# Performance work log

Hardware: AMD Instinct MI355X
Metric: run time of the kernel (lower is better)

The kernel has to match this reference:

```python
import jax, jax.numpy as jnp
import numpy as np

N_EMBD = 1024
N_HEAD = 16
HEAD_SIZE = 64

def setup_inputs() -> dict:
    key = jax.random.key(0)
    ks = jax.random.split(key, 6)
    B, T = 4, 2048
    x = jax.random.normal(ks[0], (B, T, N_EMBD), dtype=jnp.float32)
    s = 1.0 / np.sqrt(N_EMBD)
    Wq = jax.random.normal(ks[1], (N_HEAD, N_EMBD, HEAD_SIZE), dtype=jnp.float32) * s
    Wk = jax.random.normal(ks[2], (N_HEAD, N_EMBD, HEAD_SIZE), dtype=jnp.float32) * s
    Wv = jax.random.normal(ks[3], (N_HEAD, N_EMBD, HEAD_SIZE), dtype=jnp.float32) * s
    Wp = jax.random.normal(ks[4], (N_EMBD, N_EMBD), dtype=jnp.float32) * s
    bp = jax.random.normal(ks[5], (N_EMBD,), dtype=jnp.float32) * 0.01
    return {"x": x, "Wq": Wq, "Wk": Wk, "Wv": Wv, "Wp": Wp, "bp": bp}

def reference(x, Wq, Wk, Wv, Wp, bp):
    B, T, C = x.shape
    # per-head projections, all heads at once: [B,H,T,hs]
    q = jnp.einsum('btc,hcd->bhtd', x, Wq)
    k = jnp.einsum('btc,hcd->bhtd', x, Wk)
    v = jnp.einsum('btc,hcd->bhtd', x, Wv)
    # NOTE: original scales by C**-0.5 with C = n_embd (not head_size)
    scale = C ** (-0.5)
    wei = jnp.einsum('bhtd,bhsd->bhts', q, k) * scale  # [B,H,T,T]
    causal = jnp.tril(jnp.ones((T, T), dtype=bool))
    wei = jnp.where(causal, wei, -jnp.inf)
    wei = jax.nn.softmax(wei, axis=-1)
    out = jnp.einsum('bhts,bhsd->bhtd', wei, v)  # [B,H,T,hs]
    out = out.transpose(0, 2, 1, 3).reshape(B, T, -1)  # concat heads -> [B,T,C]
    return out @ Wp + bp
```

## Files before the change

kernel.cpp:

```cpp
#include <hip/hip_runtime.h>
#include <stdint.h>
#include <math.h>

typedef short s16x8 __attribute__((ext_vector_type(8)));
typedef float f32x4 __attribute__((ext_vector_type(4)));
typedef float f32x16 __attribute__((ext_vector_type(16)));

__device__ __forceinline__ unsigned short f2bf(float f) {
    union { float f; uint32_t u; } x; x.f = f;
    uint32_t r = x.u + 0x7FFFu + ((x.u >> 16) & 1u);
    return (unsigned short)(r >> 16);
}

__device__ __forceinline__ uint32_t cvtpk_bf16(float lo, float hi) {
    uint32_t r;
    asm("v_cvt_pk_bf16_f32 %0, %1, %2" : "=v"(r) : "v"(lo), "v"(hi));
    return r;
}

#define GLD_LDS16(gp, lp) __builtin_amdgcn_global_load_lds( \
    (const __attribute__((address_space(1))) uint32_t*)(gp), \
    (__attribute__((address_space(3))) uint32_t*)(lp), 16, 0, 0)

#define MFMA16x16x32(a, b, c) __builtin_amdgcn_mfma_f32_16x16x32_bf16((a), (b), (c), 0, 0, 0)
#define MFMA32x32x16(a, b, c) __builtin_amdgcn_mfma_f32_32x32x16_bf16((a), (b), (c), 0, 0, 0)

__device__ __forceinline__ void plswap(uint32_t a, uint32_t b, int lh, uint32_t& x, uint32_t& y) {
#if __has_builtin(__builtin_amdgcn_permlane32_swap)
    auto r = __builtin_amdgcn_permlane32_swap(a, b, false, false);
    x = (uint32_t)r[0]; y = (uint32_t)r[1];
#else
    uint32_t as = (uint32_t)__shfl_xor((int)a, 32, 64);
    uint32_t bs = (uint32_t)__shfl_xor((int)b, 32, 64);
    x = lh ? bs : a;
    y = lh ? b : as;
#endif
}

__global__ void cvt_all_kernel(const float* __restrict__ x,
                               const float* __restrict__ Wq, const float* __restrict__ Wk,
                               const float* __restrict__ Wv, const float* __restrict__ Wp,
                               unsigned short* __restrict__ xb,
                               unsigned short* __restrict__ WtQKV, unsigned short* __restrict__ WtP,
                               int xunits) {
    int u = blockIdx.x * blockDim.x + threadIdx.x;
    if (u < xunits) {
        int i = u * 4;
        float4 v = *(const float4*)(x + i);
        unsigned short o0 = f2bf(v.x), o1 = f2bf(v.y), o2 = f2bf(v.z), o3 = f2bf(v.w);
        uint64_t packed = (uint64_t)o0 | ((uint64_t)o1 << 16) | ((uint64_t)o2 << 32) | ((uint64_t)o3 << 48);
        *(uint64_t*)(xb + i) = packed;
        return;
    }
    int id = (u - xunits) * 4;
    int which = id >> 20, rem = id & 1048575;
    const float* src = (which == 0) ? Wq : (which == 1) ? Wk : (which == 2) ? Wv : Wp;
    float4 v = *(const float4*)(src + rem);
    unsigned short* dst;
    if (which < 3) {
        int h = rem >> 16, c = (rem >> 6) & 1023, d = rem & 63;
        dst = WtQKV + (size_t)(which * 1024 + h * 64 + d) * 1024 + c;
    } else {
        int c = rem >> 10, n = rem & 1023;
        dst = WtP + (size_t)n * 1024 + c;
    }
    dst[0] = f2bf(v.x); dst[1024] = f2bf(v.y); dst[2048] = f2bf(v.z); dst[3072] = f2bf(v.w);
}

template<int MODE, int CPX>
__global__ __launch_bounds__(512, 4) void gemm_dp_kernel(
    const unsigned short* __restrict__ A, const unsigned short* __restrict__ Bt,
    void* __restrict__ Cout, unsigned short* __restrict__ vT,
    const float* __restrict__ bias)
{
    constexpr int K = 1024, NT = 32;
    __shared__ __align__(16) unsigned short LA[3][128 * 32];
    __shared__ __align__(16) unsigned short LB[3][256 * 32];

    const int t = threadIdx.x, w = t >> 6, l = t & 63, lr = l & 15, lg = l >> 4;
    const int wm2 = w >> 2, wn4 = w & 3;

    int bid = blockIdx.x;
    int swz = (bid & 7) * CPX + (bid >> 3);
    const int bm = (swz & 63) << 7, bn = (swz >> 6) << 8;

    const unsigned short* Ab = A + (size_t)bm * K;
    const unsigned short* Bb = Bt + (size_t)bn * K;

    int sArow, sAce, sBrow[2], sBce[2];
    {
        int u = t >> 4, x = (t & 15) ^ (u & 15);
        sArow = 4 * u + (x >> 2); sAce = (x & 3) << 3;
        #pragma unroll
        for (int i2 = 0; i2 < 2; ++i2) {
            int i = t + i2 * 512;
            int ub = i >> 4, xb2 = (i & 15) ^ (ub & 15);
            sBrow[i2] = 4 * ub + (xb2 >> 2); sBce[i2] = (xb2 & 3) << 3;
        }
    }

    int aoff[4], boff[4];
    #pragma unroll
    for (int m = 0; m < 4; ++m) {
        int u = 16 * wm2 + 4 * m + (lr >> 2);
        aoff[m] = u * 256 + (((lg + 4 * (lr & 3)) ^ (u & 15)) << 4);
    }
    #pragma unroll
    for (int n = 0; n < 4; ++n) {
        int u = 16 * wn4 + 4 * n + (lr >> 2);
        boff[n] = u * 256 + (((lg + 4 * (lr & 3)) ^ (u & 15)) << 4);
    }

    f32x4 acc[4][4] = {};

    GLD_LDS16(Ab + (size_t)sArow * K + 0 + sAce, &LA[0][t * 8]);
    #pragma unroll
    for (int i2 = 0; i2 < 2; ++i2)
        GLD_LDS16(Bb + (size_t)sBrow[i2] * K + 0 + sBce[i2], &LB[0][(t + i2 * 512) * 8]);
    GLD_LDS16(Ab + (size_t)sArow * K + 32 + sAce, &LA[1][t * 8]);
    #pragma unroll
    for (int i2 = 0; i2 < 2; ++i2)
        GLD_LDS16(Bb + (size_t)sBrow[i2] * K + 32 + sBce[i2], &LB[1][(t + i2 * 512) * 8]);
    asm volatile("s_waitcnt vmcnt(3)" ::: "memory");
    __builtin_amdgcn_sched_barrier(0);
    __builtin_amdgcn_s_barrier();

    int cur = 0;
    for (int j = 0; j < NT; ++j) {
        const int dst = (cur >= 1) ? cur - 1 : cur + 2;
        const bool st = (j + 2 < NT);
        const int k2 = (j + 2) << 5;
        s16x8 af[4], bfr[4];
        #pragma unroll
        for (int m = 0; m < 4; ++m)
            af[m] = *(const s16x8*)((const char*)LA[cur] + aoff[m]);
        #pragma unroll
        for (int n = 0; n < 4; ++n)
            bfr[n] = *(const s16x8*)((const char*)LB[cur] + boff[n]);
        if (st) {
            GLD_LDS16(Ab + (size_t)sArow * K + k2 + sAce, &LA[dst][t * 8]);
            #pragma unroll
            for (int i2 = 0; i2 < 2; ++i2)
                GLD_LDS16(Bb + (size_t)sBrow[i2] * K + k2 + sBce[i2], &LB[dst][(t + i2 * 512) * 8]);
        }
        __builtin_amdgcn_s_barrier();
        asm volatile("s_waitcnt lgkmcnt(0)" ::: "memory");
        __builtin_amdgcn_sched_barrier(0);
        __builtin_amdgcn_s_setprio(1);
        #pragma unroll
        for (int m = 0; m < 4; ++m)
            #pragma unroll
            for (int n = 0; n < 4; ++n)
                acc[m][n] = MFMA16x16x32(af[m], bfr[n], acc[m][n]);
        __builtin_amdgcn_s_setprio(0);
        if (j + 1 < NT) {
            if (st) { asm volatile("s_waitcnt vmcnt(3)" ::: "memory"); }
            else    { asm volatile("s_waitcnt vmcnt(0)" ::: "memory"); }
            __builtin_amdgcn_sched_barrier(0);
        }
        __builtin_amdgcn_s_barrier();
        cur = (cur == 2) ? 0 : cur + 1;
    }

    if (MODE == 1) {
        float* C = (float*)Cout;
        #pragma unroll
        for (int mi = 0; mi < 4; ++mi)
            #pragma unroll
            for (int ni = 0; ni < 4; ++ni) {
                int col = bn + wn4 * 64 + ni * 16 + lr;
                float bv = bias[col];
                int row0 = bm + wm2 * 64 + mi * 16 + lg * 4;
                #pragma unroll
                for (int r = 0; r < 4; ++r)
                    C[(size_t)(row0 + r) * 1024 + col] = acc[mi][ni][r] + bv;
            }
    } else {
        unsigned short* qkv2 = (unsigned short*)Cout;
        const bool isV = (bn >= 2048);
        const float sc = (bn < 1024) ? (0.03125f * 1.44269504088896341f) : 1.0f;
        #pragma unroll
        for (int mi = 0; mi < 4; ++mi)
            #pragma unroll
            for (int ni = 0; ni < 4; ++ni) {
                int col = bn + wn4 * 64 + ni * 16 + lr;
                int row0 = bm + wm2 * 64 + mi * 16 + lg * 4;
                if (!isV) {
                    #pragma unroll
                    for (int r = 0; r < 4; ++r)
                        qkv2[(size_t)(row0 + r) * 2048 + col] = f2bf(acc[mi][ni][r] * sc);
                } else {
                    int h = (col >> 6) & 15, d = col & 63;
                    size_t vb = ((size_t)((row0 >> 11) * 16 + h) * 64 + d) * 2048 + (row0 & 2047);
                    uint32_t u0 = (uint32_t)f2bf(acc[mi][ni][0]) | ((uint32_t)f2bf(acc[mi][ni][1]) << 16);
                    uint32_t u1 = (uint32_t)f2bf(acc[mi][ni][2]) | ((uint32_t)f2bf(acc[mi][ni][3]) << 16);
                    *(uint32_t*)&vT[vb]     = u0;
                    *(uint32_t*)&vT[vb + 2] = u1;
                }
            }
    }
}

__device__ __forceinline__ void proc32(
    const unsigned short* __restrict__ Ksb, const unsigned short* __restrict__ Vtb,
    const s16x8* qf, f32x16* o, float& m_r, f32x16& l_acc, s16x8 onesf,
    int qms, bool domask, int lq, int lh)
{
    const int ub = lq >> 1;
    const int vb8 = (lq & 1) << 3;
    f32x16 S[2] = {};
    __builtin_amdgcn_s_setprio(1);
    #pragma unroll
    for (int sblk = 0; sblk < 2; ++sblk)
        #pragma unroll
        for (int kd = 0; kd < 4; ++kd) {
            s16x8 kf = *(const s16x8*)((const char*)Ksb + (sblk * 16 + ub) * 256
                                       + ((((2 * kd + lh) + vb8) ^ ub) << 4));
            S[sblk] = MFMA32x32x16(kf, qf[kd], S[sblk]);
        }
    __builtin_amdgcn_s_setprio(0);
    if (domask) {
        #pragma unroll
        for (int sblk = 0; sblk < 2; ++sblk)
            #pragma unroll
            for (int r = 0; r < 16; ++r) {
                int s_loc = sblk * 32 + (r & 3) + 8 * (r >> 2) + 4 * lh;
                S[sblk][r] = (s_loc <= qms) ? S[sblk][r] : -1e30f;
            }
    }
    float zm = S[0][0];
    #pragma unroll
    for (int r = 1; r < 15; r += 2) zm = fmaxf(fmaxf(zm, S[0][r]), S[0][r + 1]);
    zm = fmaxf(zm, S[0][15]);
    #pragma unroll
    for (int r = 0; r < 16; r += 2) zm = fmaxf(fmaxf(zm, S[1][r]), S[1][r + 1]);
    zm = fmaxf(zm, __shfl_xor(zm, 32, 64));
    const bool defer = (__all(zm <= m_r + 8.0f) != 0);
    if (!defer) {
        float mn = fmaxf(m_r, zm);
        float alpha = exp2f(m_r - mn);
        m_r = mn;
        l_acc[0] *= alpha;
        o[0] *= alpha;
        o[1] *= alpha;
    }
    uint32_t pk[2][8];
    #pragma unroll
    for (int sblk = 0; sblk < 2; ++sblk) {
        #pragma unroll
        for (int r = 0; r < 16; ++r)
            S[sblk][r] = exp2f(S[sblk][r] - m_r);
        #pragma unroll
        for (int hh = 0; hh < 8; ++hh)
            pk[sblk][hh] = cvtpk_bf16(S[sblk][2 * hh], S[sblk][2 * hh + 1]);
    }
    s16x8 pf[4];
    #pragma unroll
    for (int ks2 = 0; ks2 < 4; ++ks2) {
        int sb = ks2 >> 1, Bh = 4 * (ks2 & 1);
        uint32_t w0, w1, w2, w3;
        plswap(pk[sb][Bh + 0], pk[sb][Bh + 2], lh, w0, w2);
        plswap(pk[sb][Bh + 1], pk[sb][Bh + 3], lh, w1, w3);
        union { uint32_t u[4]; s16x8 v; } pu;
        pu.u[0] = w0; pu.u[1] = w1; pu.u[2] = w2; pu.u[3] = w3;
        pf[ks2] = pu.v;
    }
    __builtin_amdgcn_s_setprio(1);
    #pragma unroll
    for (int dblk = 0; dblk < 2; ++dblk)
        #pragma unroll
        for (int ks2 = 0; ks2 < 4; ++ks2) {
            s16x8 vf = *(const s16x8*)((const char*)Vtb + (dblk * 16 + ub) * 256
                                       + ((((2 * ks2 + lh) + vb8) ^ ub) << 4));
            o[dblk] = MFMA32x32x16(vf, pf[ks2], o[dblk]);
        }
    #pragma unroll
    for (int ks2 = 0; ks2 < 4; ++ks2)
        l_acc = MFMA32x32x16(onesf, pf[ks2], l_acc);
    __builtin_amdgcn_s_setprio(0);
}

__global__ __launch_bounds__(256, 4) void attn_kernel(
    const unsigned short* __restrict__ qkv2, const unsigned short* __restrict__ vT,
    unsigned short* __restrict__ attnO, int T)
{
    __shared__ __align__(16) unsigned short Ks[2][64 * 64];
    __shared__ __align__(16) unsigned short Vt[2][64 * 64];

    const int i = blockIdx.x;
    const int g = i & 7, j = i >> 3;
    const int tq = 15 - (j >> 3);
    const int bh = ((j & 7) << 3) | g;
    const int b = bh >> 4, h = bh & 15;
    const int nkv = 2 * tq + 2;

    const int t = threadIdx.x, w = t >> 6, l = t & 63, lq = l & 31, lh = l >> 5;
    const int c0 = tq * 128 + 32 * w;
    const int lastT = (c0 + 31) >> 6;

    const unsigned short* qbase = qkv2 + (size_t)b * T * 2048;
    const unsigned short* kbase = qbase + 1024 + h * 64;
    const unsigned short* vtb   = vT + (size_t)(b * 16 + h) * 64 * 2048;

    s16x8 qf[4];
    #pragma unroll
    for (int kd = 0; kd < 4; ++kd)
        qf[kd] = *(const s16x8*)(qbase + (size_t)(c0 + lq) * 2048 + h * 64 + kd * 16 + lh * 8);

    f32x16 o[2] = {}, l_acc = {};
    float m_r = -1e30f;
    s16x8 onesf;
    {
        union { uint32_t u[4]; s16x8 v; } ou;
        #pragma unroll
        for (int k2 = 0; k2 < 4; ++k2) ou.u[k2] = 0x3F803F80u;
        onesf = ou.v;
    }

    int srow[2], sch[2];
    #pragma unroll
    for (int i2 = 0; i2 < 2; ++i2) {
        int c = t + i2 * 256;
        int su = c >> 4, sx = (c & 15) ^ (su & 15);
        srow[i2] = 2 * su + (sx >> 3); sch[i2] = (sx & 7) << 3;
    }
    auto STAGE = [&](int buf, int s0) {
        #pragma unroll
        for (int i2 = 0; i2 < 2; ++i2) {
            int c = t + i2 * 256;
            GLD_LDS16(kbase + (size_t)(s0 + srow[i2]) * 2048 + sch[i2], &Ks[buf][c * 8]);
            GLD_LDS16(vtb + (size_t)srow[i2] * 2048 + s0 + sch[i2], &Vt[buf][c * 8]);
        }
    };

    STAGE(0, 0);
    __syncthreads();

    for (int kt = 0; kt < nkv; ++kt) {
        const int cur = kt & 1, nxt = cur ^ 1;
        if (kt + 1 < nkv) STAGE(nxt, (kt + 1) * 64);
        if (kt <= lastT)
            proc32(Ks[cur], Vt[cur], qf, o, m_r, l_acc, onesf,
                   c0 + lq - kt * 64, kt == lastT, lq, lh);
        __syncthreads();
    }

    {
        float inv = 1.0f / l_acc[0];
        #pragma unroll
        for (int dblk = 0; dblk < 2; ++dblk)
            #pragma unroll
            for (int r = 0; r < 16; r += 2) {
                int d = dblk * 32 + (r & 3) + 8 * (r >> 2) + 4 * lh;
                uint32_t ua = cvtpk_bf16(o[dblk][r] * inv, o[dblk][r + 1] * inv);
                *(uint32_t*)&attnO[(size_t)(b * T + c0 + lq) * 1024 + h * 64 + d] = ua;
            }
    }
}

extern "C" void kernel_launch(void* const* d_in, const int* in_sizes, int n_in,
                              void* d_out, int out_size, void* d_ws, size_t ws_size,
                              hipStream_t stream) {
    const float* x  = (const float*)d_in[0];
    const float* Wq = (const float*)d_in[1];
    const float* Wk = (const float*)d_in[2];
    const float* Wv = (const float*)d_in[3];
    const float* Wp = (const float*)d_in[4];
    const float* bp = (const float*)d_in[5];
    float* out = (float*)d_out;

    const int T = 2048, C = 1024;
    const int BT = in_sizes[0] / C;
    const int B  = BT / T;

    char* ws = (char*)d_ws;
    unsigned short* xb    = (unsigned short*)(ws);
    unsigned short* WtQKV = (unsigned short*)(ws + 16777216);
    unsigned short* WtP   = (unsigned short*)(ws + 23068672);
    unsigned short* qkv2  = (unsigned short*)(ws + 25165824);
    unsigned short* vT    = (unsigned short*)(ws + 58720256);
    unsigned short* attn  = (unsigned short*)(ws + 75497472);
    (void)ws_size; (void)n_in; (void)out_size;

    const int xunits = BT * C / 4;
    const int wunits = 4 * 1024 * 1024 / 4;
    cvt_all_kernel<<<(xunits + wunits) / 256, 256, 0, stream>>>(
        x, Wq, Wk, Wv, Wp, xb, WtQKV, WtP, xunits);

    gemm_dp_kernel<0, 96><<<768, 512, 0, stream>>>(xb, WtQKV, qkv2, vT, nullptr);

    attn_kernel<<<B * 16 * 16, 256, 0, stream>>>(qkv2, vT, attn, T);

    gemm_dp_kernel<1, 32><<<256, 512, 0, stream>>>(attn, WtP, out, nullptr, bp);
}
```

Baseline: 198.4 us.

## Split attention KV tiles across wave pairs and merge partial softmax states

Each block now handles 64 queries instead of 128, so the grid doubles. Each pair of waves splits the 64-key tile into two 32-key halves, each half keeping its own running max and sum, and the halves are merged through LDS at the end. The row-sum MFMA against a ones vector is replaced by a scalar sum with a lane shuffle, and the occupancy hint rises from 4 to 5. This aims to cut causal load imbalance and per-tile MFMA work, at the cost of loading each K/V tile twice as often overall and adding an LDS merge epilogue.

```diff
diff --git a/kernel.cpp b/kernel.cpp
--- a/kernel.cpp
+++ b/kernel.cpp
@@ -201,102 +201,94 @@
     }
 }
 
-__device__ __forceinline__ void proc32(
+__device__ __forceinline__ void proc32h(
     const unsigned short* __restrict__ Ksb, const unsigned short* __restrict__ Vtb,
-    const s16x8* qf, f32x16* o, float& m_r, f32x16& l_acc, s16x8 onesf,
-    int qms, bool domask, int lq, int lh)
+    const s16x8* qf, f32x16* o, float& m_r, float& l_r,
+    int qms, bool domask, int lq, int lh, int wp)
 {
     const int ub = lq >> 1;
     const int vb8 = (lq & 1) << 3;
-    f32x16 S[2] = {};
+    f32x16 S = {};
     __builtin_amdgcn_s_setprio(1);
     #pragma unroll
-    for (int sblk = 0; sblk < 2; ++sblk)
-        #pragma unroll
-        for (int kd = 0; kd < 4; ++kd) {
-            s16x8 kf = *(const s16x8*)((const char*)Ksb + (sblk * 16 + ub) * 256
-                                       + ((((2 * kd + lh) + vb8) ^ ub) << 4));
-            S[sblk] = MFMA32x32x16(kf, qf[kd], S[sblk]);
-        }
+    for (int kd = 0; kd < 4; ++kd) {
+        s16x8 kf = *(const s16x8*)((const char*)Ksb + (wp * 16 + ub) * 256
+                                   + ((((2 * kd + lh) + vb8) ^ ub) << 4));
+        S = MFMA32x32x16(kf, qf[kd], S);
+    }
     __builtin_amdgcn_s_setprio(0);
     if (domask) {
         #pragma unroll
-        for (int sblk = 0; sblk < 2; ++sblk)
-            #pragma unroll
-            for (int r = 0; r < 16; ++r) {
-                int s_loc = sblk * 32 + (r & 3) + 8 * (r >> 2) + 4 * lh;
-                S[sblk][r] = (s_loc <= qms) ? S[sblk][r] : -1e30f;
-            }
-    }
-    float zm = S[0][0];
-    #pragma unroll
-    for (int r = 1; r < 15; r += 2) zm = fmaxf(fmaxf(zm, S[0][r]), S[0][r + 1]);
-    zm = fmaxf(zm, S[0][15]);
-    #pragma unroll
-    for (int r = 0; r < 16; r += 2) zm = fmaxf(fmaxf(zm, S[1][r]), S[1][r + 1]);
+        for (int r = 0; r < 16; ++r) {
+            int s_loc = (r & 3) + 8 * (r >> 2) + 4 * lh;
+            S[r] = (s_loc <= qms) ? S[r] : -1e30f;
+        }
+    }
+    float zm = fmaxf(S[0], S[1]);
+    #pragma unroll
+    for (int r = 2; r < 16; r += 2) zm = fmaxf(fmaxf(zm, S[r]), S[r + 1]);
     zm = fmaxf(zm, __shfl_xor(zm, 32, 64));
     const bool defer = (__all(zm <= m_r + 8.0f) != 0);
     if (!defer) {
         float mn = fmaxf(m_r, zm);
         float alpha = exp2f(m_r - mn);
         m_r = mn;
-        l_acc[0] *= alpha;
+        l_r *= alpha;
         o[0] *= alpha;
         o[1] *= alpha;
     }
-    uint32_t pk[2][8];
-    #pragma unroll
-    for (int sblk = 0; sblk < 2; ++sblk) {
-        #pragma unroll
-        for (int r = 0; r < 16; ++r)
-            S[sblk][r] = exp2f(S[sblk][r] - m_r);
-        #pragma unroll
-        for (int hh = 0; hh < 8; ++hh)
-            pk[sblk][hh] = cvtpk_bf16(S[sblk][2 * hh], S[sblk][2 * hh + 1]);
-    }
-    s16x8 pf[4];
-    #pragma unroll
-    for (int ks2 = 0; ks2 < 4; ++ks2) {
-        int sb = ks2 >> 1, Bh = 4 * (ks2 & 1);
+    float rs = 0.0f;
+    uint32_t pk[8];
+    #pragma unroll
+    for (int r = 0; r < 16; ++r) {
+        float pv = exp2f(S[r] - m_r);
+        S[r] = pv;
+        rs += pv;
+    }
+    #pragma unroll
+    for (int hh = 0; hh < 8; ++hh)
+        pk[hh] = cvtpk_bf16(S[2 * hh], S[2 * hh + 1]);
+    rs += __shfl_xor(rs, 32, 64);
+    l_r += rs;
+    s16x8 pf[2];
+    #pragma unroll
+    for (int jj = 0; jj < 2; ++jj) {
         uint32_t w0, w1, w2, w3;
-        plswap(pk[sb][Bh + 0], pk[sb][Bh + 2], lh, w0, w2);
-        plswap(pk[sb][Bh + 1], pk[sb][Bh + 3], lh, w1, w3);
+        plswap(pk[4 * jj + 0], pk[4 * jj + 2], lh, w0, w2);
+        plswap(pk[4 * jj + 1], pk[4 * jj + 3], lh, w1, w3);
         union { uint32_t u[4]; s16x8 v; } pu;
         pu.u[0] = w0; pu.u[1] = w1; pu.u[2] = w2; pu.u[3] = w3;
-        pf[ks2] = pu.v;
+        pf[jj] = pu.v;
     }
     __builtin_amdgcn_s_setprio(1);
     #pragma unroll
     for (int dblk = 0; dblk < 2; ++dblk)
         #pragma unroll
-        for (int ks2 = 0; ks2 < 4; ++ks2) {
+        for (int jj = 0; jj < 2; ++jj) {
+            int kc = 2 * (2 * wp + jj) + lh;
             s16x8 vf = *(const s16x8*)((const char*)Vtb + (dblk * 16 + ub) * 256
-                                       + ((((2 * ks2 + lh) + vb8) ^ ub) << 4));
-            o[dblk] = MFMA32x32x16(vf, pf[ks2], o[dblk]);
-        }
-    #pragma unroll
-    for (int ks2 = 0; ks2 < 4; ++ks2)
-        l_acc = MFMA32x32x16(onesf, pf[ks2], l_acc);
+                                       + (((kc + vb8) ^ ub) << 4));
+            o[dblk] = MFMA32x32x16(vf, pf[jj], o[dblk]);
+        }
     __builtin_amdgcn_s_setprio(0);
 }
 
-__global__ __launch_bounds__(256, 4) void attn_kernel(
+__global__ __launch_bounds__(256, 5) void attn_kernel(
     const unsigned short* __restrict__ qkv2, const unsigned short* __restrict__ vT,
     unsigned short* __restrict__ attnO, int T)
 {
-    __shared__ __align__(16) unsigned short Ks[2][64 * 64];
-    __shared__ __align__(16) unsigned short Vt[2][64 * 64];
+    __shared__ __align__(16) unsigned short SMEM[4][64 * 64];
 
     const int i = blockIdx.x;
     const int g = i & 7, j = i >> 3;
-    const int tq = 15 - (j >> 3);
+    const int tq = 31 - (j >> 3);
     const int bh = ((j & 7) << 3) | g;
     const int b = bh >> 4, h = bh & 15;
-    const int nkv = 2 * tq + 2;
+    const int nkv = tq + 1;
 
     const int t = threadIdx.x, w = t >> 6, l = t & 63, lq = l & 31, lh = l >> 5;
-    const int c0 = tq * 128 + 32 * w;
-    const int lastT = (c0 + 31) >> 6;
+    const int ws = w & 1, wp = w >> 1;
+    const int c0 = tq * 64 + 32 * ws;
 
     const unsigned short* qbase = qkv2 + (size_t)b * T * 2048;
     const unsigned short* kbase = qbase + 1024 + h * 64;
@@ -307,15 +299,8 @@
     for (int kd = 0; kd < 4; ++kd)
         qf[kd] = *(const s16x8*)(qbase + (size_t)(c0 + lq) * 2048 + h * 64 + kd * 16 + lh * 8);
 
-    f32x16 o[2] = {}, l_acc = {};
-    float m_r = -1e30f;
-    s16x8 onesf;
-    {
-        union { uint32_t u[4]; s16x8 v; } ou;
-        #pragma unroll
-        for (int k2 = 0; k2 < 4; ++k2) ou.u[k2] = 0x3F803F80u;
-        onesf = ou.v;
-    }
+    f32x16 o[2] = {};
+    float m_r = -1e30f, l_r = 0.0f;
 
     int srow[2], sch[2];
     #pragma unroll
@@ -328,8 +313,8 @@
         #pragma unroll
         for (int i2 = 0; i2 < 2; ++i2) {
             int c = t + i2 * 256;
-            GLD_LDS16(kbase + (size_t)(s0 + srow[i2]) * 2048 + sch[i2], &Ks[buf][c * 8]);
-            GLD_LDS16(vtb + (size_t)srow[i2] * 2048 + s0 + sch[i2], &Vt[buf][c * 8]);
+            GLD_LDS16(kbase + (size_t)(s0 + srow[i2]) * 2048 + sch[i2], &SMEM[buf][c * 8]);
+            GLD_LDS16(vtb + (size_t)srow[i2] * 2048 + s0 + sch[i2], &SMEM[2 + buf][c * 8]);
         }
     };
 
@@ -339,20 +324,41 @@
     for (int kt = 0; kt < nkv; ++kt) {
         const int cur = kt & 1, nxt = cur ^ 1;
         if (kt + 1 < nkv) STAGE(nxt, (kt + 1) * 64);
-        if (kt <= lastT)
-            proc32(Ks[cur], Vt[cur], qf, o, m_r, l_acc, onesf,
-                   c0 + lq - kt * 64, kt == lastT, lq, lh);
+        const int sbase = 64 * kt + 32 * wp;
+        if (sbase <= c0 + 31)
+            proc32h(SMEM[cur], SMEM[2 + cur], qf, o, m_r, l_r,
+                    c0 + lq - sbase, sbase + 31 > c0, lq, lh, wp);
         __syncthreads();
     }
 
-    {
-        float inv = 1.0f / l_acc[0];
+    float* fs = (float*)&SMEM[0][0];
+    if (lh == 0) { fs[w * 64 + lq * 2] = m_r; fs[w * 64 + lq * 2 + 1] = l_r; }
+    __syncthreads();
+    float m_o = fs[(w ^ 2) * 64 + lq * 2], l_o = fs[(w ^ 2) * 64 + lq * 2 + 1];
+    float M = fmaxf(m_r, m_o);
+    float s_self = exp2f(m_r - M);
+    float s_oth  = exp2f(m_o - M);
+    float L = l_r * s_self + l_o * s_oth;
+    float fsc = s_self / L;
+    __syncthreads();
+    float* cb = fs + ws * 2048;
+    if (wp == 1) {
         #pragma unroll
         for (int dblk = 0; dblk < 2; ++dblk)
             #pragma unroll
+            for (int r = 0; r < 16; ++r)
+                cb[(dblk * 16 + r) * 64 + lq * 2 + lh] = o[dblk][r] * fsc;
+    }
+    __syncthreads();
+    if (wp == 0) {
+        #pragma unroll
+        for (int dblk = 0; dblk < 2; ++dblk)
+            #pragma unroll
             for (int r = 0; r < 16; r += 2) {
+                float v0 = o[dblk][r] * fsc     + cb[(dblk * 16 + r) * 64 + lq * 2 + lh];
+                float v1 = o[dblk][r + 1] * fsc + cb[(dblk * 16 + r + 1) * 64 + lq * 2 + lh];
                 int d = dblk * 32 + (r & 3) + 8 * (r >> 2) + 4 * lh;
-                uint32_t ua = cvtpk_bf16(o[dblk][r] * inv, o[dblk][r + 1] * inv);
+                uint32_t ua = cvtpk_bf16(v0, v1);
                 *(uint32_t*)&attnO[(size_t)(b * T + c0 + lq) * 1024 + h * 64 + d] = ua;
             }
     }
@@ -389,7 +395,7 @@
 
     gemm_dp_kernel<0, 96><<<768, 512, 0, stream>>>(xb, WtQKV, qkv2, vT, nullptr);
 
-    attn_kernel<<<B * 16 * 16, 256, 0, stream>>>(qkv2, vT, attn, T);
+    attn_kernel<<<B * 16 * 32, 256, 0, stream>>>(qkv2, vT, attn, T);
 
     gemm_dp_kernel<1, 32><<<256, 512, 0, stream>>>(attn, WtP, out, nullptr, bp);
 }
```

New measurement: 193.4 us (median of 2 runs). 2.5% less time.
